# Optimization experiments

Hardware: AMD Instinct MI355X
Metric: run time of the kernel (lower is better)

Reference implementation:

```python
import jax, jax.numpy as jnp
import numpy as np

B, S, D, H = 2, 2048, 1024, 16
HD = D // H  # head dim = 64

def setup_inputs() -> dict:
    key = jax.random.key(0)
    k1, k2, k3, k4, k5 = jax.random.split(key, 5)
    return {
        "x": jax.random.normal(k1, (B, S, D), dtype=jnp.float32),
        "w_qkv": jax.random.normal(k2, (D, 3 * D), dtype=jnp.float32) * (1.0 / np.sqrt(D)),
        "b_qkv": jax.random.normal(k3, (3 * D,), dtype=jnp.float32) * 0.02,
        "w_out": jax.random.normal(k4, (D, D), dtype=jnp.float32) * (1.0 / np.sqrt(D)),
        "b_out": jax.random.normal(k5, (D,), dtype=jnp.float32) * 0.02,
        "c": 0,
    }

def reference(x, w_qkv, b_qkv, w_out, b_out, c):
    # fused QKV projection: [B,S,3D]
    qkv = jnp.einsum('bsd,de->bse', x, w_qkv) + b_qkv
    q, k, v = jnp.split(qkv, 3, axis=-1)
    # [B,S,D] -> [B,H,S,HD]
    split_heads = lambda t: t.reshape(B, S, H, HD).transpose(0, 2, 1, 3)
    q, k, v = split_heads(q), split_heads(k), split_heads(v)
    scale = 1.0 / np.sqrt(HD).astype(np.float32)
    scores = jnp.einsum('bhqd,bhkd->bhqk', q, k) * scale  # [B,H,S,S]
    probs = jax.nn.softmax(scores, axis=-1)
    # c==1 noise path references an undefined `const` in the original (dead/broken);
    # dropout probs are 0 -> identity (eval mode).
    attn = jnp.einsum('bhqk,bhkd->bhqd', probs, v)  # [B,H,S,HD]
    attn = attn.transpose(0, 2, 1, 3).reshape(B, S, D)
    out = jnp.einsum('bsd,de->bse', attn, w_out) + b_out
    return out
```

## Files before the change

### kernel.cpp

```cpp
#include <hip/hip_runtime.h>


typedef __attribute__((ext_vector_type(8))) short bs8;
typedef __attribute__((ext_vector_type(4))) short bs4;
typedef __attribute__((ext_vector_type(4))) float f32x4;

__device__ __forceinline__ f32x4 MFMA16K16(bs4 a, bs4 b, f32x4 c) {
#if defined(__HIP_DEVICE_COMPILE__)
  return __builtin_amdgcn_mfma_f32_16x16x16bf16_1k(a, b, c, 0, 0, 0);
#else
  return c;
#endif
}

#define QSCALE 0.18033688011112042f
#define MBOUND 24.0f

__device__ __forceinline__ unsigned short f2bf(float f) {
  union { float f; unsigned int u; } v; v.f = f;
  return (unsigned short)((v.u + 0x8000u) >> 16);
}

__device__ __forceinline__ unsigned int pkbf2(float a, float b) {
  union { float f; unsigned int u; } va, vb; va.f = a; vb.f = b;
#if defined(__HIP_DEVICE_COMPILE__)
  return __builtin_amdgcn_perm(vb.u + 0x8000u, va.u + 0x8000u, 0x07060302u);
#else
  return 0u;
#endif
}

__device__ __forceinline__ void async16(const unsigned short* g, unsigned short* lds) {
  __builtin_amdgcn_global_load_lds(
      (const __attribute__((address_space(1))) unsigned int*)g,
      (__attribute__((address_space(3))) unsigned int*)lds, 16, 0, 0);
}

__device__ __forceinline__ void stage_rows64(unsigned short* lds, const unsigned short* src,
                                             int ldk, int w, int l) {
#pragma unroll
  for (int i = 0; i < 4; ++i) {
    int row = (w * 4 + i) * 8 + (l >> 3);
    int cg  = (l & 7) ^ (l >> 3);
    async16(src + (size_t)row * ldk + cg * 8, lds + (w * 4 + i) * 512);
  }
}

__device__ __forceinline__ void stage_rows64_8w(unsigned short* lds, const unsigned short* src,
                                                int ldk, int w, int l) {
#pragma unroll
  for (int i = 0; i < 2; ++i) {
    int row = (w * 2 + i) * 8 + (l >> 3);
    int cg  = (l & 7) ^ (l >> 3);
    async16(src + (size_t)row * ldk + cg * 8, lds + (w * 2 + i) * 512);
  }
}

__device__ __forceinline__ void stage_vt_8w(unsigned short* lds, const unsigned short* vtb,
                                            int keyofs, int w, int l) {
#pragma unroll
  for (int i = 0; i < 2; ++i) {
    int row = (w * 2 + i) * 4 + (l >> 4);
    int cg = (l & 15) ^ (row & 15);
    async16(vtb + (size_t)row * 2048 + keyofs + cg * 8, lds + (w * 2 + i) * 512);
  }
}

__device__ __forceinline__ void transpose_cast_body(const float* __restrict__ src,
                                                    unsigned short* __restrict__ dst,
                                                    int R, int C, int bx, int by, int t) {
  __shared__ unsigned short tile[64][73];
  int c0 = bx * 64, r0 = by * 64;
  int rl = t >> 2, cb = (t & 3) * 16;
  const float* p = src + (size_t)(r0 + rl) * C + c0 + cb;
#pragma unroll
  for (int j = 0; j < 16; j += 4) {
    float4 f = *(const float4*)(p + j);
    tile[rl][cb + j + 0] = f2bf(f.x);
    tile[rl][cb + j + 1] = f2bf(f.y);
    tile[rl][cb + j + 2] = f2bf(f.z);
    tile[rl][cb + j + 3] = f2bf(f.w);
  }
  __syncthreads();
  int cl = t >> 2, rb = (t & 3) * 16;
  unsigned short* q = dst + (size_t)(c0 + cl) * R + r0 + rb;
#pragma unroll
  for (int j = 0; j < 16; ++j) q[j] = tile[rb + j][cl];
}

__global__ __launch_bounds__(256) void prep_kernel(const float* __restrict__ x,
                                                   unsigned short* __restrict__ xb,
                                                   const float* __restrict__ w_qkv,
                                                   unsigned short* __restrict__ wt1,
                                                   const float* __restrict__ w_out,
                                                   unsigned short* __restrict__ wt2) {
  int blk = blockIdx.x, t = threadIdx.x;
  if (blk < 2048) {
    int i = (blk * 256 + t) * 8;
    float4 a = *(const float4*)(x + i);
    float4 b = *(const float4*)(x + i + 4);
    union { bs8 v; unsigned short u[8]; } o;
    o.u[0] = f2bf(a.x); o.u[1] = f2bf(a.y); o.u[2] = f2bf(a.z); o.u[3] = f2bf(a.w);
    o.u[4] = f2bf(b.x); o.u[5] = f2bf(b.y); o.u[6] = f2bf(b.z); o.u[7] = f2bf(b.w);
    *(bs8*)(xb + i) = o.v;
  } else if (blk < 2816) {
    int i = blk - 2048;
    transpose_cast_body(w_qkv, wt1, 1024, 3072, i % 48, i / 48, t);
  } else {
    int i = blk - 2816;
    transpose_cast_body(w_out, wt2, 1024, 1024, i % 16, i / 16, t);
  }
}

__global__ __launch_bounds__(256) void gemm_qkv_kernel(const unsigned short* __restrict__ A,
                                                       const unsigned short* __restrict__ Bt,
                                                       const float* __restrict__ bias,
                                                       unsigned short* __restrict__ qo,
                                                       unsigned short* __restrict__ ko,
                                                       unsigned short* __restrict__ vto) {
  __shared__ unsigned short As[128 * 64];
  __shared__ unsigned short Bs[128 * 64];
  int t = threadIdx.x, w = t >> 6, l = t & 63;
  int m16 = l & 15, q = l >> 4;
  int wm = w >> 1, wn = w & 1;
  int bm = blockIdx.y, bn = blockIdx.x;
  bool vsec = (bn >= 16);
  const unsigned short* Abase = A + (size_t)bm * 128 * 1024;
  const unsigned short* Bbase = Bt + (size_t)bn * 128 * 1024;
  f32x4 zero4 = {0.f, 0.f, 0.f, 0.f};
  f32x4 acc[4][4];
#pragma unroll
  for (int i = 0; i < 4; ++i)
#pragma unroll
    for (int j = 0; j < 4; ++j) acc[i][j] = zero4;
  for (int kt = 0; kt < 16; ++kt) {
    stage_rows64(As, Abase + kt * 64, 1024, w, l);
    stage_rows64(Bs, Bbase + kt * 64, 1024, w, l);
    __syncthreads();
#pragma unroll
    for (int ks = 0; ks < 2; ++ks) {
      bs8 af[4], bf[4];
#pragma unroll
      for (int mt = 0; mt < 4; ++mt) {
        int row = wm * 64 + mt * 16 + m16;
        int c = ks * 4 + q;
        af[mt] = *(const bs8*)&As[row * 64 + ((c ^ (row & 7)) * 8)];
      }
#pragma unroll
      for (int nt = 0; nt < 4; ++nt) {
        int row = wn * 64 + nt * 16 + m16;
        int c = ks * 4 + q;
        bf[nt] = *(const bs8*)&Bs[row * 64 + ((c ^ (row & 7)) * 8)];
      }
      if (vsec) {
#pragma unroll
        for (int mt = 0; mt < 4; ++mt)
#pragma unroll
          for (int nt = 0; nt < 4; ++nt)
            acc[mt][nt] = __builtin_amdgcn_mfma_f32_16x16x32_bf16(af[mt], bf[nt],
                                                                  acc[mt][nt], 0, 0, 0);
      } else {
#pragma unroll
        for (int mt = 0; mt < 4; ++mt)
#pragma unroll
          for (int nt = 0; nt < 4; ++nt)
            acc[mt][nt] = __builtin_amdgcn_mfma_f32_16x16x32_bf16(bf[nt], af[mt],
                                                                  acc[mt][nt], 0, 0, 0);
      }
    }
    __syncthreads();
  }
  if (!vsec) {
#pragma unroll
    for (int nt = 0; nt < 4; ++nt) {
      int ng0 = bn * 128 + wn * 64 + nt * 16 + q * 4;
      float4 bb = *(const float4*)&bias[ng0];
      int sect = ng0 >> 10;
      unsigned short* dst = sect ? ko : qo;
      float sc = sect ? 1.0f : QSCALE;
      int f0 = ng0 & 1023, h = f0 >> 6, hd0 = f0 & 63;
#pragma unroll
      for (int mt = 0; mt < 4; ++mt) {
        int mg = bm * 128 + wm * 64 + mt * 16 + m16;
        int b = mg >> 11, s = mg & 2047;
        union { bs4 v; unsigned short u[4]; } pv;
        pv.u[0] = f2bf((acc[mt][nt][0] + bb.x) * sc);
        pv.u[1] = f2bf((acc[mt][nt][1] + bb.y) * sc);
        pv.u[2] = f2bf((acc[mt][nt][2] + bb.z) * sc);
        pv.u[3] = f2bf((acc[mt][nt][3] + bb.w) * sc);
        *(bs4*)&dst[((size_t)(b * 16 + h) * 2048 + s) * 64 + hd0] = pv.v;
      }
    }
  } else {
#pragma unroll
    for (int nt = 0; nt < 4; ++nt) {
      int ng = bn * 128 + wn * 64 + nt * 16 + m16;
      float bb = bias[ng];
      int f = ng & 1023, h = f >> 6, hd = f & 63;
      int sw4 = (hd & 8) ? 4 : 0;
#pragma unroll
      for (int mt = 0; mt < 4; ++mt) {
        int mg0 = bm * 128 + wm * 64 + mt * 16 + q * 4;
        int b = mg0 >> 11, s0 = (mg0 & 2047) ^ sw4;
        union { bs4 v; unsigned short u[4]; } pv;
#pragma unroll
        for (int r = 0; r < 4; ++r) pv.u[r] = f2bf(acc[mt][nt][r] + bb);
        *(bs4*)&vto[((size_t)(b * 16 + h) * 64 + hd) * 2048 + s0] = pv.v;
      }
    }
  }
}

__global__ __launch_bounds__(256) void gemm_out_kernel(const unsigned short* __restrict__ A,
                                                       const unsigned short* __restrict__ Bt,
                                                       const float* __restrict__ bias,
                                                       float* __restrict__ out) {
  __shared__ unsigned short As[64 * 64];
  __shared__ unsigned short Bs[128 * 64];
  int t = threadIdx.x, w = t >> 6, l = t & 63;
  int m16 = l & 15, q = l >> 4;
  int wm = w >> 1, wn = w & 1;
  int bm = blockIdx.y, bn = blockIdx.x;
  const unsigned short* Abase = A + (size_t)bm * 64 * 1024;
  const unsigned short* Bbase = Bt + (size_t)bn * 128 * 1024;
  f32x4 zero4 = {0.f, 0.f, 0.f, 0.f};
  f32x4 acc[2][4];
#pragma unroll
  for (int i = 0; i < 2; ++i)
#pragma unroll
    for (int j = 0; j < 4; ++j) acc[i][j] = zero4;
  for (int kt = 0; kt < 16; ++kt) {
    stage_rows64_8w(As, Abase + kt * 64, 1024, w, l);
    stage_rows64(Bs, Bbase + kt * 64, 1024, w, l);
    __syncthreads();
#pragma unroll
    for (int ks = 0; ks < 2; ++ks) {
      bs8 af[2], bf[4];
#pragma unroll
      for (int mt = 0; mt < 2; ++mt) {
        int row = wm * 32 + mt * 16 + m16;
        int c = ks * 4 + q;
        af[mt] = *(const bs8*)&As[row * 64 + ((c ^ (row & 7)) * 8)];
      }
#pragma unroll
      for (int nt = 0; nt < 4; ++nt) {
        int row = wn * 64 + nt * 16 + m16;
        int c = ks * 4 + q;
        bf[nt] = *(const bs8*)&Bs[row * 64 + ((c ^ (row & 7)) * 8)];
      }
#pragma unroll
      for (int mt = 0; mt < 2; ++mt)
#pragma unroll
        for (int nt = 0; nt < 4; ++nt)
          acc[mt][nt] = __builtin_amdgcn_mfma_f32_16x16x32_bf16(bf[nt], af[mt],
                                                                acc[mt][nt], 0, 0, 0);
    }
    __syncthreads();
  }
#pragma unroll
  for (int nt = 0; nt < 4; ++nt) {
    int ng0 = bn * 128 + wn * 64 + nt * 16 + q * 4;
    float4 bb = *(const float4*)&bias[ng0];
#pragma unroll
    for (int mt = 0; mt < 2; ++mt) {
      int mg = bm * 64 + wm * 32 + mt * 16 + m16;
      float4 ov;
      ov.x = acc[mt][nt][0] + bb.x;
      ov.y = acc[mt][nt][1] + bb.y;
      ov.z = acc[mt][nt][2] + bb.z;
      ov.w = acc[mt][nt][3] + bb.w;
      *(float4*)&out[(size_t)mg * 1024 + ng0] = ov;
    }
  }
}

__global__ __launch_bounds__(512, 4) void attn_kernel(const unsigned short* __restrict__ Q,
                                                      const unsigned short* __restrict__ K,
                                                      const unsigned short* __restrict__ Vt,
                                                      unsigned short* __restrict__ Aout) {
  __shared__ unsigned short Ks[2][128 * 64];
  __shared__ unsigned short Vts[2][64 * 128];
  int t = threadIdx.x, w = t >> 6, l = t & 63;
  int m16 = l & 15, q = l >> 4;
  int wq = w & 3, kh = w >> 2;
  int qt = blockIdx.x, bh = blockIdx.y;
  const unsigned short* qbase = Q + (size_t)bh * 2048 * 64 + (size_t)qt * 128 * 64;
  const unsigned short* kbase = K + (size_t)bh * 2048 * 64;
  const unsigned short* vtbase = Vt + (size_t)bh * 64 * 2048;

  bs8 qf[2][2];
#pragma unroll
  for (int mt = 0; mt < 2; ++mt)
#pragma unroll
    for (int ks = 0; ks < 2; ++ks)
      qf[mt][ks] = *(const bs8*)(qbase + (size_t)(wq * 32 + mt * 16 + m16) * 64 + ks * 32 + q * 8);

  stage_rows64_8w(&Ks[0][0], kbase, 64, w, l);
  stage_vt_8w(&Vts[0][0], vtbase, 0, w, l);
  __syncthreads();

  f32x4 minit = {-MBOUND, -MBOUND, -MBOUND, -MBOUND};
  f32x4 zero4 = {0.f, 0.f, 0.f, 0.f};
  f32x4 o[2][4];
  float lsum[2] = {0.f, 0.f};
#pragma unroll
  for (int mt = 0; mt < 2; ++mt)
#pragma unroll
    for (int nh = 0; nh < 4; ++nh) o[mt][nh] = zero4;

  int vsw = (m16 >> 3) & 1;

  for (int kt = 0; kt < 16; ++kt) {
    int buf = kt & 1;
    if (kt < 15) {
      stage_rows64_8w(&Ks[buf ^ 1][0], kbase + (size_t)(kt + 1) * 128 * 64, 64, w, l);
      stage_vt_8w(&Vts[buf ^ 1][0], vtbase, (kt + 1) * 128, w, l);
    }
    const unsigned short* Kb = &Ks[buf][0];
    const unsigned short* Vb = &Vts[buf][0];

    f32x4 sAcc[2][4];
#pragma unroll
    for (int mt = 0; mt < 2; ++mt)
#pragma unroll
      for (int nt = 0; nt < 4; ++nt) sAcc[mt][nt] = minit;
#pragma unroll
    for (int ks = 0; ks < 2; ++ks) {
      bs8 kf[4];
#pragma unroll
      for (int nt = 0; nt < 4; ++nt) {
        int row = kh * 64 + nt * 16 + m16;
        int c = ks * 4 + q;
        kf[nt] = *(const bs8*)&Kb[row * 64 + ((c ^ (row & 7)) * 8)];
      }
#pragma unroll
      for (int nt = 0; nt < 4; ++nt)
#pragma unroll
        for (int mt = 0; mt < 2; ++mt)
          sAcc[mt][nt] = __builtin_amdgcn_mfma_f32_16x16x32_bf16(kf[nt], qf[mt][ks],
                                                                 sAcc[mt][nt], 0, 0, 0);
    }

#pragma unroll
    for (int mt = 0; mt < 2; ++mt) {
      float rs = 0.f;
#pragma unroll
      for (int nt = 0; nt < 4; ++nt)
#pragma unroll
        for (int r = 0; r < 4; ++r) {
          float p = __builtin_amdgcn_exp2f(sAcc[mt][nt][r]);
          sAcc[mt][nt][r] = p;
          rs += p;
        }
      lsum[mt] += rs;
    }

#pragma unroll
    for (int nt = 0; nt < 4; ++nt) {
      bs4 vf[4];
#pragma unroll
      for (int nh = 0; nh < 4; ++nh) {
        int vrow = nh * 16 + m16;
        int chunk = kh * 8 + nt * 2 + (q >> 1);
        int within = ((q & 1) ^ vsw) * 4;
        vf[nh] = *(const bs4*)&Vb[vrow * 128 + ((chunk ^ (vrow & 15)) * 8) + within];
      }
#pragma unroll
      for (int mt = 0; mt < 2; ++mt) {
        union { bs4 v; unsigned int u[2]; } pf;
        pf.u[0] = pkbf2(sAcc[mt][nt][0], sAcc[mt][nt][1]);
        pf.u[1] = pkbf2(sAcc[mt][nt][2], sAcc[mt][nt][3]);
#pragma unroll
        for (int nh = 0; nh < 4; ++nh)
          o[mt][nh] = MFMA16K16(vf[nh], pf.v, o[mt][nh]);
      }
    }
    __syncthreads();
  }

  float* ored = (float*)&Ks[0][0];
  float* lred = (float*)&Vts[0][0];
  if (w >= 4) {
#pragma unroll
    for (int mt = 0; mt < 2; ++mt)
#pragma unroll
      for (int nh = 0; nh < 4; ++nh)
        *(f32x4*)&ored[((mt * 4 + nh) * 256 + wq * 64 + l) * 4] = o[mt][nh];
    lred[0 * 256 + wq * 64 + l] = lsum[0];
    lred[1 * 256 + wq * 64 + l] = lsum[1];
  }
  __syncthreads();
  if (w < 4) {
#pragma unroll
    for (int mt = 0; mt < 2; ++mt)
#pragma unroll
      for (int nh = 0; nh < 4; ++nh) {
        f32x4 part = *(const f32x4*)&ored[((mt * 4 + nh) * 256 + wq * 64 + l) * 4];
#pragma unroll
        for (int r = 0; r < 4; ++r) o[mt][nh][r] += part[r];
      }
    lsum[0] += lred[0 * 256 + wq * 64 + l];
    lsum[1] += lred[1 * 256 + wq * 64 + l];

    int b = bh >> 4, h = bh & 15;
#pragma unroll
    for (int mt = 0; mt < 2; ++mt) {
      float l0 = lsum[mt];
      l0 += __shfl_xor(l0, 16);
      l0 += __shfl_xor(l0, 32);
      float inv = 1.0f / l0;
      int s = qt * 128 + wq * 32 + mt * 16 + m16;
#pragma unroll
      for (int nh = 0; nh < 4; ++nh)
#pragma unroll
        for (int r = 0; r < 4; ++r) {
          int hd = nh * 16 + q * 4 + r;
          Aout[((size_t)(b * 2048 + s)) * 1024 + h * 64 + hd] = f2bf(o[mt][nh][r] * inv);
        }
    }
  }
}

extern "C" void kernel_launch(void* const* d_in, const int* in_sizes, int n_in,
                              void* d_out, int out_size, void* d_ws, size_t ws_size,
                              hipStream_t stream) {
  const float* x     = (const float*)d_in[0];
  const float* w_qkv = (const float*)d_in[1];
  const float* b_qkv = (const float*)d_in[2];
  const float* w_out = (const float*)d_in[3];
  const float* b_out = (const float*)d_in[4];
  float* out = (float*)d_out;

  char* ws = (char*)d_ws;
  unsigned short* xb    = (unsigned short*)(ws);
  unsigned short* wt1   = (unsigned short*)(ws + (8u << 20));
  unsigned short* wt2   = (unsigned short*)(ws + (14u << 20));
  unsigned short* qb    = (unsigned short*)(ws + (16u << 20));
  unsigned short* kb    = (unsigned short*)(ws + (24u << 20));
  unsigned short* vtb   = (unsigned short*)(ws + (32u << 20));
  unsigned short* attnb = (unsigned short*)(ws + (40u << 20));

  prep_kernel<<<3072, 256, 0, stream>>>(x, xb, w_qkv, wt1, w_out, wt2);
  gemm_qkv_kernel<<<dim3(24, 32), 256, 0, stream>>>(xb, wt1, b_qkv, qb, kb, vtb);
  attn_kernel<<<dim3(16, 32), 512, 0, stream>>>(qb, kb, vtb, attnb);
  gemm_out_kernel<<<dim3(8, 64), 256, 0, stream>>>(attnb, wt2, b_out, out);
}
```

Baseline: 186.7 us.

## Shrink attention tiles to 64 queries and 64 keys with 4-wave blocks

```diff
diff --git a/kernel.cpp b/kernel.cpp
--- a/kernel.cpp
+++ b/kernel.cpp
@@ -53,16 +53,6 @@
     int row = (w * 2 + i) * 8 + (l >> 3);
     int cg  = (l & 7) ^ (l >> 3);
     async16(src + (size_t)row * ldk + cg * 8, lds + (w * 2 + i) * 512);
-  }
-}
-
-__device__ __forceinline__ void stage_vt_8w(unsigned short* lds, const unsigned short* vtb,
-                                            int keyofs, int w, int l) {
-#pragma unroll
-  for (int i = 0; i < 2; ++i) {
-    int row = (w * 2 + i) * 4 + (l >> 4);
-    int cg = (l & 15) ^ (row & 15);
-    async16(vtb + (size_t)row * 2048 + keyofs + cg * 8, lds + (w * 2 + i) * 512);
   }
 }
 
@@ -274,17 +264,17 @@
   }
 }
 
-__global__ __launch_bounds__(512, 4) void attn_kernel(const unsigned short* __restrict__ Q,
+__global__ __launch_bounds__(256, 4) void attn_kernel(const unsigned short* __restrict__ Q,
                                                       const unsigned short* __restrict__ K,
                                                       const unsigned short* __restrict__ Vt,
                                                       unsigned short* __restrict__ Aout) {
-  __shared__ unsigned short Ks[2][128 * 64];
-  __shared__ unsigned short Vts[2][64 * 128];
+  __shared__ unsigned short Ks[2][64 * 64];
+  __shared__ unsigned short Vts[2][64 * 64];
   int t = threadIdx.x, w = t >> 6, l = t & 63;
   int m16 = l & 15, q = l >> 4;
-  int wq = w & 3, kh = w >> 2;
+  int wq = w & 1, kh = w >> 1;
   int qt = blockIdx.x, bh = blockIdx.y;
-  const unsigned short* qbase = Q + (size_t)bh * 2048 * 64 + (size_t)qt * 128 * 64;
+  const unsigned short* qbase = Q + (size_t)bh * 2048 * 64 + (size_t)qt * 64 * 64;
   const unsigned short* kbase = K + (size_t)bh * 2048 * 64;
   const unsigned short* vtbase = Vt + (size_t)bh * 64 * 2048;
 
@@ -296,7 +286,7 @@
       qf[mt][ks] = *(const bs8*)(qbase + (size_t)(wq * 32 + mt * 16 + m16) * 64 + ks * 32 + q * 8);
 
   stage_rows64_8w(&Ks[0][0], kbase, 64, w, l);
-  stage_vt_8w(&Vts[0][0], vtbase, 0, w, l);
+  stage_rows64_8w(&Vts[0][0], vtbase, 2048, w, l);
   __syncthreads();
 
   f32x4 minit = {-MBOUND, -MBOUND, -MBOUND, -MBOUND};
@@ -310,42 +300,45 @@
 
   int vsw = (m16 >> 3) & 1;
 
-  for (int kt = 0; kt < 16; ++kt) {
+#pragma unroll 2
+  for (int kt = 0; kt < 32; ++kt) {
     int buf = kt & 1;
-    if (kt < 15) {
-      stage_rows64_8w(&Ks[buf ^ 1][0], kbase + (size_t)(kt + 1) * 128 * 64, 64, w, l);
-      stage_vt_8w(&Vts[buf ^ 1][0], vtbase, (kt + 1) * 128, w, l);
+    if (kt < 31) {
+      stage_rows64_8w(&Ks[buf ^ 1][0], kbase + (size_t)(kt + 1) * 64 * 64, 64, w, l);
+      stage_rows64_8w(&Vts[buf ^ 1][0], vtbase + (kt + 1) * 64, 2048, w, l);
     }
     const unsigned short* Kb = &Ks[buf][0];
     const unsigned short* Vb = &Vts[buf][0];
 
-    f32x4 sAcc[2][4];
+    f32x4 sAcc[2][2];
 #pragma unroll
     for (int mt = 0; mt < 2; ++mt)
 #pragma unroll
-      for (int nt = 0; nt < 4; ++nt) sAcc[mt][nt] = minit;
+      for (int nt = 0; nt < 2; ++nt) sAcc[mt][nt] = minit;
 #pragma unroll
     for (int ks = 0; ks < 2; ++ks) {
-      bs8 kf[4];
-#pragma unroll
-      for (int nt = 0; nt < 4; ++nt) {
-        int row = kh * 64 + nt * 16 + m16;
+      bs8 kf[2];
+#pragma unroll
+      for (int nt = 0; nt < 2; ++nt) {
+        int row = kh * 32 + nt * 16 + m16;
         int c = ks * 4 + q;
         kf[nt] = *(const bs8*)&Kb[row * 64 + ((c ^ (row & 7)) * 8)];
       }
-#pragma unroll
-      for (int nt = 0; nt < 4; ++nt)
+      __builtin_amdgcn_s_setprio(1);
+#pragma unroll
+      for (int nt = 0; nt < 2; ++nt)
 #pragma unroll
         for (int mt = 0; mt < 2; ++mt)
           sAcc[mt][nt] = __builtin_amdgcn_mfma_f32_16x16x32_bf16(kf[nt], qf[mt][ks],
                                                                  sAcc[mt][nt], 0, 0, 0);
+      __builtin_amdgcn_s_setprio(0);
     }
 
 #pragma unroll
     for (int mt = 0; mt < 2; ++mt) {
       float rs = 0.f;
 #pragma unroll
-      for (int nt = 0; nt < 4; ++nt)
+      for (int nt = 0; nt < 2; ++nt)
 #pragma unroll
         for (int r = 0; r < 4; ++r) {
           float p = __builtin_amdgcn_exp2f(sAcc[mt][nt][r]);
@@ -356,23 +349,25 @@
     }
 
 #pragma unroll
-    for (int nt = 0; nt < 4; ++nt) {
+    for (int nt = 0; nt < 2; ++nt) {
       bs4 vf[4];
 #pragma unroll
       for (int nh = 0; nh < 4; ++nh) {
         int vrow = nh * 16 + m16;
-        int chunk = kh * 8 + nt * 2 + (q >> 1);
+        int g = kh * 4 + nt * 2 + (q >> 1);
         int within = ((q & 1) ^ vsw) * 4;
-        vf[nh] = *(const bs4*)&Vb[vrow * 128 + ((chunk ^ (vrow & 15)) * 8) + within];
+        vf[nh] = *(const bs4*)&Vb[vrow * 64 + ((g ^ (vrow & 7)) * 8) + within];
       }
 #pragma unroll
       for (int mt = 0; mt < 2; ++mt) {
         union { bs4 v; unsigned int u[2]; } pf;
         pf.u[0] = pkbf2(sAcc[mt][nt][0], sAcc[mt][nt][1]);
         pf.u[1] = pkbf2(sAcc[mt][nt][2], sAcc[mt][nt][3]);
+        __builtin_amdgcn_s_setprio(1);
 #pragma unroll
         for (int nh = 0; nh < 4; ++nh)
           o[mt][nh] = MFMA16K16(vf[nh], pf.v, o[mt][nh]);
+        __builtin_amdgcn_s_setprio(0);
       }
     }
     __syncthreads();
@@ -380,27 +375,27 @@
 
   float* ored = (float*)&Ks[0][0];
   float* lred = (float*)&Vts[0][0];
-  if (w >= 4) {
+  if (kh == 1) {
 #pragma unroll
     for (int mt = 0; mt < 2; ++mt)
 #pragma unroll
       for (int nh = 0; nh < 4; ++nh)
-        *(f32x4*)&ored[((mt * 4 + nh) * 256 + wq * 64 + l) * 4] = o[mt][nh];
-    lred[0 * 256 + wq * 64 + l] = lsum[0];
-    lred[1 * 256 + wq * 64 + l] = lsum[1];
+        *(f32x4*)&ored[((mt * 4 + nh) * 128 + wq * 64 + l) * 4] = o[mt][nh];
+    lred[0 * 128 + wq * 64 + l] = lsum[0];
+    lred[1 * 128 + wq * 64 + l] = lsum[1];
   }
   __syncthreads();
-  if (w < 4) {
+  if (kh == 0) {
 #pragma unroll
     for (int mt = 0; mt < 2; ++mt)
 #pragma unroll
       for (int nh = 0; nh < 4; ++nh) {
-        f32x4 part = *(const f32x4*)&ored[((mt * 4 + nh) * 256 + wq * 64 + l) * 4];
+        f32x4 part = *(const f32x4*)&ored[((mt * 4 + nh) * 128 + wq * 64 + l) * 4];
 #pragma unroll
         for (int r = 0; r < 4; ++r) o[mt][nh][r] += part[r];
       }
-    lsum[0] += lred[0 * 256 + wq * 64 + l];
-    lsum[1] += lred[1 * 256 + wq * 64 + l];
+    lsum[0] += lred[0 * 128 + wq * 64 + l];
+    lsum[1] += lred[1 * 128 + wq * 64 + l];
 
     int b = bh >> 4, h = bh & 15;
 #pragma unroll
@@ -409,14 +404,14 @@
       l0 += __shfl_xor(l0, 16);
       l0 += __shfl_xor(l0, 32);
       float inv = 1.0f / l0;
-      int s = qt * 128 + wq * 32 + mt * 16 + m16;
-#pragma unroll
-      for (int nh = 0; nh < 4; ++nh)
-#pragma unroll
-        for (int r = 0; r < 4; ++r) {
-          int hd = nh * 16 + q * 4 + r;
-          Aout[((size_t)(b * 2048 + s)) * 1024 + h * 64 + hd] = f2bf(o[mt][nh][r] * inv);
-        }
+      int s = qt * 64 + wq * 32 + mt * 16 + m16;
+#pragma unroll
+      for (int nh = 0; nh < 4; ++nh) {
+        union { bs4 v; unsigned short u[4]; } pv;
+#pragma unroll
+        for (int r = 0; r < 4; ++r) pv.u[r] = f2bf(o[mt][nh][r] * inv);
+        *(bs4*)&Aout[((size_t)(b * 2048 + s)) * 1024 + h * 64 + nh * 16 + q * 4] = pv.v;
+      }
     }
   }
 }
@@ -442,6 +437,6 @@
 
   prep_kernel<<<3072, 256, 0, stream>>>(x, xb, w_qkv, wt1, w_out, wt2);
   gemm_qkv_kernel<<<dim3(24, 32), 256, 0, stream>>>(xb, wt1, b_qkv, qb, kb, vtb);
-  attn_kernel<<<dim3(16, 32), 512, 0, stream>>>(qb, kb, vtb, attnb);
+  attn_kernel<<<dim3(32, 32), 256, 0, stream>>>(qb, kb, vtb, attnb);
   gemm_out_kernel<<<dim3(8, 64), 256, 0, stream>>>(attnb, wt2, b_out, out);
 }
```

New measurement: 195.6 us. 4.8% more time.

## Switch attention kernel to 32x32x16 MFMA tiles with permlane32 P repacking

Applied to the files above, without the earlier changes.

```diff
diff --git a/kernel.cpp b/kernel.cpp
--- a/kernel.cpp
+++ b/kernel.cpp
@@ -4,14 +4,7 @@
 typedef __attribute__((ext_vector_type(8))) short bs8;
 typedef __attribute__((ext_vector_type(4))) short bs4;
 typedef __attribute__((ext_vector_type(4))) float f32x4;
-
-__device__ __forceinline__ f32x4 MFMA16K16(bs4 a, bs4 b, f32x4 c) {
-#if defined(__HIP_DEVICE_COMPILE__)
-  return __builtin_amdgcn_mfma_f32_16x16x16bf16_1k(a, b, c, 0, 0, 0);
-#else
-  return c;
-#endif
-}
+typedef __attribute__((ext_vector_type(16))) float f32x16;
 
 #define QSCALE 0.18033688011112042f
 #define MBOUND 24.0f
@@ -27,6 +20,12 @@
   return __builtin_amdgcn_perm(vb.u + 0x8000u, va.u + 0x8000u, 0x07060302u);
 #else
   return 0u;
+#endif
+}
+
+__device__ __forceinline__ void pls32(unsigned int &a, unsigned int &b) {
+#if defined(__HIP_DEVICE_COMPILE__)
+  asm("v_permlane32_swap_b32 %0, %1" : "+v"(a), "+v"(b));
 #endif
 }
 
@@ -197,11 +196,10 @@
       int ng = bn * 128 + wn * 64 + nt * 16 + m16;
       float bb = bias[ng];
       int f = ng & 1023, h = f >> 6, hd = f & 63;
-      int sw4 = (hd & 8) ? 4 : 0;
 #pragma unroll
       for (int mt = 0; mt < 4; ++mt) {
         int mg0 = bm * 128 + wm * 64 + mt * 16 + q * 4;
-        int b = mg0 >> 11, s0 = (mg0 & 2047) ^ sw4;
+        int b = mg0 >> 11, s0 = mg0 & 2047;
         union { bs4 v; unsigned short u[4]; } pv;
 #pragma unroll
         for (int r = 0; r < 4; ++r) pv.u[r] = f2bf(acc[mt][nt][r] + bb);
@@ -281,34 +279,29 @@
   __shared__ unsigned short Ks[2][128 * 64];
   __shared__ unsigned short Vts[2][64 * 128];
   int t = threadIdx.x, w = t >> 6, l = t & 63;
-  int m16 = l & 15, q = l >> 4;
+  int c32 = l & 31, lh = l >> 5;
   int wq = w & 3, kh = w >> 2;
   int qt = blockIdx.x, bh = blockIdx.y;
   const unsigned short* qbase = Q + (size_t)bh * 2048 * 64 + (size_t)qt * 128 * 64;
   const unsigned short* kbase = K + (size_t)bh * 2048 * 64;
   const unsigned short* vtbase = Vt + (size_t)bh * 64 * 2048;
 
-  bs8 qf[2][2];
-#pragma unroll
-  for (int mt = 0; mt < 2; ++mt)
-#pragma unroll
-    for (int ks = 0; ks < 2; ++ks)
-      qf[mt][ks] = *(const bs8*)(qbase + (size_t)(wq * 32 + mt * 16 + m16) * 64 + ks * 32 + q * 8);
+  bs8 qf[4];
+#pragma unroll
+  for (int ks = 0; ks < 4; ++ks)
+    qf[ks] = *(const bs8*)(qbase + (size_t)(wq * 32 + c32) * 64 + ks * 16 + lh * 8);
 
   stage_rows64_8w(&Ks[0][0], kbase, 64, w, l);
   stage_vt_8w(&Vts[0][0], vtbase, 0, w, l);
   __syncthreads();
 
-  f32x4 minit = {-MBOUND, -MBOUND, -MBOUND, -MBOUND};
-  f32x4 zero4 = {0.f, 0.f, 0.f, 0.f};
-  f32x4 o[2][4];
-  float lsum[2] = {0.f, 0.f};
-#pragma unroll
-  for (int mt = 0; mt < 2; ++mt)
-#pragma unroll
-    for (int nh = 0; nh < 4; ++nh) o[mt][nh] = zero4;
-
-  int vsw = (m16 >> 3) & 1;
+  f32x16 sAcc[2];
+  f32x16 o[2];
+  float lsum = 0.f;
+#pragma unroll
+  for (int nh = 0; nh < 2; ++nh)
+#pragma unroll
+    for (int r = 0; r < 16; ++r) o[nh][r] = 0.f;
 
   for (int kt = 0; kt < 16; ++kt) {
     int buf = kt & 1;
@@ -319,60 +312,53 @@
     const unsigned short* Kb = &Ks[buf][0];
     const unsigned short* Vb = &Vts[buf][0];
 
-    f32x4 sAcc[2][4];
-#pragma unroll
-    for (int mt = 0; mt < 2; ++mt)
-#pragma unroll
-      for (int nt = 0; nt < 4; ++nt) sAcc[mt][nt] = minit;
-#pragma unroll
-    for (int ks = 0; ks < 2; ++ks) {
-      bs8 kf[4];
-#pragma unroll
-      for (int nt = 0; nt < 4; ++nt) {
-        int row = kh * 64 + nt * 16 + m16;
-        int c = ks * 4 + q;
-        kf[nt] = *(const bs8*)&Kb[row * 64 + ((c ^ (row & 7)) * 8)];
-      }
-#pragma unroll
-      for (int nt = 0; nt < 4; ++nt)
-#pragma unroll
-        for (int mt = 0; mt < 2; ++mt)
-          sAcc[mt][nt] = __builtin_amdgcn_mfma_f32_16x16x32_bf16(kf[nt], qf[mt][ks],
-                                                                 sAcc[mt][nt], 0, 0, 0);
-    }
-
-#pragma unroll
-    for (int mt = 0; mt < 2; ++mt) {
+#pragma unroll
+    for (int tile = 0; tile < 2; ++tile)
+#pragma unroll
+      for (int r = 0; r < 16; ++r) sAcc[tile][r] = -MBOUND;
+#pragma unroll
+    for (int ks = 0; ks < 4; ++ks) {
+      int row0 = kh * 64 + c32;
+      int row1 = row0 + 32;
+      int cgr = ks * 2 + lh;
+      bs8 kf0 = *(const bs8*)&Kb[row0 * 64 + ((cgr ^ (row0 & 7)) * 8)];
+      bs8 kf1 = *(const bs8*)&Kb[row1 * 64 + ((cgr ^ (row1 & 7)) * 8)];
+      __builtin_amdgcn_s_setprio(1);
+      sAcc[0] = __builtin_amdgcn_mfma_f32_32x32x16_bf16(kf0, qf[ks], sAcc[0], 0, 0, 0);
+      sAcc[1] = __builtin_amdgcn_mfma_f32_32x32x16_bf16(kf1, qf[ks], sAcc[1], 0, 0, 0);
+      __builtin_amdgcn_s_setprio(0);
+    }
+
+#pragma unroll
+    for (int tile = 0; tile < 2; ++tile) {
       float rs = 0.f;
-#pragma unroll
-      for (int nt = 0; nt < 4; ++nt)
-#pragma unroll
-        for (int r = 0; r < 4; ++r) {
-          float p = __builtin_amdgcn_exp2f(sAcc[mt][nt][r]);
-          sAcc[mt][nt][r] = p;
-          rs += p;
+      unsigned int wp[8];
+#pragma unroll
+      for (int ri = 0; ri < 8; ++ri) {
+        float p0 = __builtin_amdgcn_exp2f(sAcc[tile][2 * ri]);
+        float p1 = __builtin_amdgcn_exp2f(sAcc[tile][2 * ri + 1]);
+        rs += p0 + p1;
+        wp[ri] = pkbf2(p0, p1);
+      }
+      lsum += rs;
+#pragma unroll
+      for (int kp = 0; kp < 2; ++kp) {
+        int ks2 = tile * 2 + kp;
+        unsigned int W0 = wp[kp * 4 + 0], W2 = wp[kp * 4 + 2];
+        unsigned int W1 = wp[kp * 4 + 1], W3 = wp[kp * 4 + 3];
+        pls32(W0, W2);
+        pls32(W1, W3);
+        union { bs8 v; unsigned int u[4]; } pf;
+        pf.u[0] = W0; pf.u[1] = W1; pf.u[2] = W2; pf.u[3] = W3;
+        __builtin_amdgcn_s_setprio(1);
+#pragma unroll
+        for (int nh = 0; nh < 2; ++nh) {
+          int vrow = nh * 32 + c32;
+          int gk = kh * 8 + ks2 * 2 + lh;
+          bs8 vf = *(const bs8*)&Vb[vrow * 128 + ((gk ^ (vrow & 15)) * 8)];
+          o[nh] = __builtin_amdgcn_mfma_f32_32x32x16_bf16(vf, pf.v, o[nh], 0, 0, 0);
         }
-      lsum[mt] += rs;
-    }
-
-#pragma unroll
-    for (int nt = 0; nt < 4; ++nt) {
-      bs4 vf[4];
-#pragma unroll
-      for (int nh = 0; nh < 4; ++nh) {
-        int vrow = nh * 16 + m16;
-        int chunk = kh * 8 + nt * 2 + (q >> 1);
-        int within = ((q & 1) ^ vsw) * 4;
-        vf[nh] = *(const bs4*)&Vb[vrow * 128 + ((chunk ^ (vrow & 15)) * 8) + within];
-      }
-#pragma unroll
-      for (int mt = 0; mt < 2; ++mt) {
-        union { bs4 v; unsigned int u[2]; } pf;
-        pf.u[0] = pkbf2(sAcc[mt][nt][0], sAcc[mt][nt][1]);
-        pf.u[1] = pkbf2(sAcc[mt][nt][2], sAcc[mt][nt][3]);
-#pragma unroll
-        for (int nh = 0; nh < 4; ++nh)
-          o[mt][nh] = MFMA16K16(vf[nh], pf.v, o[mt][nh]);
+        __builtin_amdgcn_s_setprio(0);
       }
     }
     __syncthreads();
@@ -380,44 +366,45 @@
 
   float* ored = (float*)&Ks[0][0];
   float* lred = (float*)&Vts[0][0];
-  if (w >= 4) {
-#pragma unroll
-    for (int mt = 0; mt < 2; ++mt)
-#pragma unroll
-      for (int nh = 0; nh < 4; ++nh)
-        *(f32x4*)&ored[((mt * 4 + nh) * 256 + wq * 64 + l) * 4] = o[mt][nh];
-    lred[0 * 256 + wq * 64 + l] = lsum[0];
-    lred[1 * 256 + wq * 64 + l] = lsum[1];
+  if (kh == 1) {
+#pragma unroll
+    for (int nh = 0; nh < 2; ++nh)
+#pragma unroll
+      for (int c = 0; c < 4; ++c) {
+        f32x4 t4 = { o[nh][c * 4 + 0], o[nh][c * 4 + 1],
+                     o[nh][c * 4 + 2], o[nh][c * 4 + 3] };
+        *(f32x4*)&ored[((nh * 4 + c) * 256 + wq * 64 + l) * 4] = t4;
+      }
+    lred[wq * 64 + l] = lsum;
   }
   __syncthreads();
-  if (w < 4) {
-#pragma unroll
-    for (int mt = 0; mt < 2; ++mt)
-#pragma unroll
-      for (int nh = 0; nh < 4; ++nh) {
-        f32x4 part = *(const f32x4*)&ored[((mt * 4 + nh) * 256 + wq * 64 + l) * 4];
-#pragma unroll
-        for (int r = 0; r < 4; ++r) o[mt][nh][r] += part[r];
-      }
-    lsum[0] += lred[0 * 256 + wq * 64 + l];
-    lsum[1] += lred[1 * 256 + wq * 64 + l];
-
-    int b = bh >> 4, h = bh & 15;
-#pragma unroll
-    for (int mt = 0; mt < 2; ++mt) {
-      float l0 = lsum[mt];
-      l0 += __shfl_xor(l0, 16);
-      l0 += __shfl_xor(l0, 32);
-      float inv = 1.0f / l0;
-      int s = qt * 128 + wq * 32 + mt * 16 + m16;
-#pragma unroll
-      for (int nh = 0; nh < 4; ++nh)
-#pragma unroll
-        for (int r = 0; r < 4; ++r) {
-          int hd = nh * 16 + q * 4 + r;
-          Aout[((size_t)(b * 2048 + s)) * 1024 + h * 64 + hd] = f2bf(o[mt][nh][r] * inv);
-        }
-    }
+  if (kh == 0) {
+#pragma unroll
+    for (int nh = 0; nh < 2; ++nh)
+#pragma unroll
+      for (int c = 0; c < 4; ++c) {
+        f32x4 part = *(const f32x4*)&ored[((nh * 4 + c) * 256 + wq * 64 + l) * 4];
+#pragma unroll
+        for (int r = 0; r < 4; ++r) o[nh][c * 4 + r] += part[r];
+      }
+    lsum += lred[wq * 64 + l];
+
+    float l0 = lsum;
+    l0 += __shfl_xor(l0, 32);
+    float inv = 1.0f / l0;
+
+    int b = bh >> 4, hh = bh & 15;
+    int s = qt * 128 + wq * 32 + c32;
+#pragma unroll
+    for (int nh = 0; nh < 2; ++nh)
+#pragma unroll
+      for (int rg = 0; rg < 4; ++rg) {
+        union { bs4 v; unsigned short u[4]; } pv;
+#pragma unroll
+        for (int r = 0; r < 4; ++r) pv.u[r] = f2bf(o[nh][rg * 4 + r] * inv);
+        int hd0 = nh * 32 + rg * 8 + 4 * lh;
+        *(bs4*)&Aout[((size_t)(b * 2048 + s)) * 1024 + hh * 64 + hd0] = pv.v;
+      }
   }
 }
 
```

Result: slower. 194.1 us (+4.0%).
